# Kernel tuning notes

Hardware: AMD Instinct MI355X
Metric: run time of the kernel (lower is better)

Reference implementation:

```python
import jax, jax.numpy as jnp
import numpy as np


def _softsign(x):
    return x / (1.0 + jnp.abs(x))


def _pad_conv3d(x, w, b):
    # replicate-pad by 1 on each spatial side, then VALID 3x3x3 conv (NCDHW)
    x = jnp.pad(x, ((0, 0), (0, 0), (1, 1), (1, 1), (1, 1)), mode='edge')
    y = jax.lax.conv_general_dilated(
        x, w, window_strides=(1, 1, 1), padding='VALID',
        dimension_numbers=('NCDHW', 'OIDHW', 'NCDHW'))
    return y + b[None, :, None, None, None]


N_MID = 100  # number of 1->1 conv blocks


def setup_inputs() -> dict:
    key = jax.random.key(0)
    ks = jax.random.split(key, 8)
    B, S = 16, 64
    preop = jax.random.normal(ks[0], (B, 1, S, S, S), dtype=jnp.float32)
    intraop = jax.random.normal(ks[1], (B, 1, S, S, S), dtype=jnp.float32)
    # conv weights: PyTorch-style kaiming-ish scale for 3x3x3 kernels
    w0 = jax.random.normal(ks[2], (1, 2, 3, 3, 3), dtype=jnp.float32) * 0.14
    b0 = jax.random.normal(ks[3], (1,), dtype=jnp.float32) * 0.05
    ws = jax.random.normal(ks[4], (N_MID, 1, 1, 3, 3, 3), dtype=jnp.float32) * 0.19
    bs = jax.random.normal(ks[5], (N_MID, 1), dtype=jnp.float32) * 0.05
    wX = jax.random.normal(ks[6], (3, 1, 3, 3, 3), dtype=jnp.float32) * 0.19
    bX = jax.random.normal(ks[7], (3,), dtype=jnp.float32) * 0.05
    return {"preoperative": preop, "intraoperative": intraop,
            "w0": w0, "b0": b0, "ws": ws, "bs": bs, "wX": wX, "bX": bX}


def reference(preoperative, intraoperative, w0, b0, ws, bs, wX, bX):
    config = jnp.concatenate((preoperative, intraoperative), axis=1)  # [B,2,D,H,W]
    h = _softsign(_pad_conv3d(config, w0, b0))  # [B,1,64,64,64]

    def step(h, wb):
        w, b = wb
        return _softsign(_pad_conv3d(h, w, b)), None

    h, _ = jax.lax.scan(step, h, (ws, bs))  # 100 chained 1->1 conv blocks
    res64 = _softsign(_pad_conv3d(h, wX, bX))  # [B,3,64,64,64]
    # torch F.interpolate default mode='nearest': src = floor(dst * in/out)
    res32 = res64[:, :, ::2, ::2, ::2]
    res16 = res64[:, :, ::4, ::4, ::4]
    res8 = res64[:, :, ::8, ::8, ::8]
    return (res64, res32, res16, res8)
```

## Files before the change

### kernel.cpp

```cpp
#include <hip/hip_runtime.h>
#include <math.h>

typedef float f4u __attribute__((ext_vector_type(4), aligned(4)));
typedef float nfloat4 __attribute__((ext_vector_type(4), aligned(16)));
typedef _Float16 h16;
typedef _Float16 h4 __attribute__((ext_vector_type(4)));
typedef _Float16 h2 __attribute__((ext_vector_type(2)));

__device__ __forceinline__ float softsign(float v) {
    float d = 1.0f + fabsf(v);
    return v * __builtin_amdgcn_rcpf(d);
}
__device__ __forceinline__ void nt_store4(float* p, float a, float b, float c, float d) {
    nfloat4 v; v.x = a; v.y = b; v.z = c; v.w = d;
    __builtin_nontemporal_store(v, (nfloat4*)p);
}
__device__ __forceinline__ int clamp63(int v) { return v < 0 ? 0 : (v > 63 ? 63 : v); }

__global__ __launch_bounds__(256) void conv_first(const float* __restrict__ in0,
                                                  const float* __restrict__ in1,
                                                  h16* __restrict__ out,
                                                  const float* __restrict__ w,
                                                  const float* __restrict__ bias) {
    int tid = blockIdx.x * 256 + threadIdx.x;
    int xq = (tid & 15) << 2;
    int y  = (tid >> 4) & 63;
    int z0 = ((tid >> 10) & 15) << 2;
    int b  = tid >> 14;
    const float* base0 = in0 + (size_t)b * 262144;
    const float* base1 = in1 + (size_t)b * 262144;

    float acc[4][4];
    #pragma unroll
    for (int i = 0; i < 4; ++i)
        #pragma unroll
        for (int j = 0; j < 4; ++j) acc[i][j] = 0.0f;

    #pragma unroll
    for (int zi = 0; zi < 6; ++zi) {
        int zin = clamp63(z0 + zi - 1);
        const float* p0 = base0 + zin * 4096;
        const float* p1 = base1 + zin * 4096;
        #pragma unroll
        for (int dy = 0; dy < 3; ++dy) {
            int yin = clamp63(y + dy - 1);
            const float* r0p = p0 + yin * 64;
            const float* r1p = p1 + yin * 64;
            float r0[6], r1[6];
            {
                const float4 v = *(const float4*)(r0p + xq);
                r0[0] = r0p[xq == 0 ? 0 : xq - 1];
                r0[1] = v.x; r0[2] = v.y; r0[3] = v.z; r0[4] = v.w;
                r0[5] = r0p[xq == 60 ? 63 : xq + 4];
            }
            {
                const float4 v = *(const float4*)(r1p + xq);
                r1[0] = r1p[xq == 0 ? 0 : xq - 1];
                r1[1] = v.x; r1[2] = v.y; r1[3] = v.z; r1[4] = v.w;
                r1[5] = r1p[xq == 60 ? 63 : xq + 4];
            }
            #pragma unroll
            for (int dz = 0; dz < 3; ++dz) {
                int zo = zi - dz;
                if (zo >= 0 && zo < 4) {
                    #pragma unroll
                    for (int dx = 0; dx < 3; ++dx) {
                        float w0v = w[dz * 9 + dy * 3 + dx];
                        float w1v = w[27 + dz * 9 + dy * 3 + dx];
                        #pragma unroll
                        for (int xx = 0; xx < 4; ++xx) {
                            acc[zo][xx] = fmaf(w0v, r0[xx + dx], acc[zo][xx]);
                            acc[zo][xx] = fmaf(w1v, r1[xx + dx], acc[zo][xx]);
                        }
                    }
                }
            }
        }
    }
    float bv = *bias;
    h16* obase = out + (size_t)b * 262144 + (size_t)z0 * 4096 + y * 64 + xq;
    #pragma unroll
    for (int zo = 0; zo < 4; ++zo) {
        h4 o;
        o.x = (h16)softsign(acc[zo][0] + bv);
        o.y = (h16)softsign(acc[zo][1] + bv);
        o.z = (h16)softsign(acc[zo][2] + bv);
        o.w = (h16)softsign(acc[zo][3] + bv);
        *(h4*)(obase + zo * 4096) = o;
    }
}

#define LROWH   68
#define LPLANEH 680

__global__ __launch_bounds__(256, 4) void conv_mid(const h16* __restrict__ in,
                                                   h16* __restrict__ out,
                                                   const float* __restrict__ w,
                                                   const float* __restrict__ bias) {
    __shared__ h16 lds[10 * LPLANEH];

    int blk = blockIdx.x;
    int xcd = blk & 7;
    int j   = blk >> 3;
    int b   = j & 15;
    int y0  = ((j >> 4) & 7) << 3;
    int z0  = xcd << 3;

    int t = threadIdx.x;
    int l = t & 15;
    int g = t >> 4;

    const h16* base = in + (size_t)b * 262144;

    float wv[27];
    #pragma unroll
    for (int i = 0; i < 27; ++i) wv[i] = w[i];
    float bv = *bias;

    {
        h16* lrows[7]; h4 mv[7]; h16 tv[7];
        #pragma unroll
        for (int it = 0; it < 7; ++it) {
            int rid = it * 16 + g;
            int pa = rid / 10;
            pa = pa > 9 ? 9 : pa;
            int pr = rid - pa * 10;
            pr = pr > 9 ? 9 : pr;
            const h16* grow = base + clamp63(z0 - 1 + pa) * 4096 + clamp63(y0 - 1 + pr) * 64;
            lrows[it] = &lds[pa * LPLANEH + pr * LROWH];
            mv[it] = *(const h4*)(grow + 4 * l);
            tv[it] = grow[63];
        }
        #pragma unroll
        for (int it = 0; it < 7; ++it) {
            int rid = it * 16 + g;
            if (rid < 100) {
                *(h4*)(lrows[it] + 4 * l) = mv[it];
                if (l == 15) { h2 d; d.x = tv[it]; d.y = tv[it]; *(h2*)(lrows[it] + 64) = d; }
            }
        }
    }
    __syncthreads();

    int xq   = l << 2;
    int yloc = g & 7;
    int zh   = (g >> 3) << 2;

    float acc[4][4];
    #pragma unroll
    for (int i = 0; i < 4; ++i)
        #pragma unroll
        for (int k = 0; k < 4; ++k) acc[i][k] = 0.0f;

    #pragma unroll
    for (int pp = 0; pp < 6; ++pp) {
        const h16* pl = &lds[(zh + pp) * LPLANEH];
        #pragma unroll
        for (int dy = 0; dy < 3; ++dy) {
            const h16* lrow = pl + (yloc + dy) * LROWH;
            h4 v  = *(const h4*)(lrow + xq);
            h2 v2 = *(const h2*)(lrow + xq + 4);
            h2 vf = *(const h2*)(lrow + (xq == 0 ? 0 : xq - 2));
            float r[6];
            r[0] = (xq == 0) ? (float)v.x : (float)vf.y;
            r[1] = (float)v.x; r[2] = (float)v.y; r[3] = (float)v.z;
            r[4] = (float)v.w; r[5] = (float)v2.x;
            #pragma unroll
            for (int dz = 0; dz < 3; ++dz) {
                int zz = pp - dz;
                if (zz >= 0 && zz < 4) {
                    #pragma unroll
                    for (int dx = 0; dx < 3; ++dx) {
                        float ww = wv[dz * 9 + dy * 3 + dx];
                        #pragma unroll
                        for (int xx = 0; xx < 4; ++xx)
                            acc[zz][xx] = fmaf(ww, r[xx + dx], acc[zz][xx]);
                    }
                }
            }
        }
    }

    int y = y0 + yloc;
    h16* obase = out + (size_t)b * 262144 + (size_t)(z0 + zh) * 4096 + y * 64 + xq;
    #pragma unroll
    for (int zz = 0; zz < 4; ++zz) {
        h4 o;
        o.x = (h16)softsign(acc[zz][0] + bv);
        o.y = (h16)softsign(acc[zz][1] + bv);
        o.z = (h16)softsign(acc[zz][2] + bv);
        o.w = (h16)softsign(acc[zz][3] + bv);
        *(h4*)(obase + zz * 4096) = o;
    }
}

__device__ __forceinline__ void load_row6h(const h16* __restrict__ row, int x0, float r[6]) {
    h4 v = *(const h4*)(row + x0);
    r[0] = (float)row[x0 == 0 ? 0 : x0 - 1];
    r[1] = (float)v.x; r[2] = (float)v.y; r[3] = (float)v.z; r[4] = (float)v.w;
    r[5] = (float)row[x0 == 60 ? 63 : x0 + 4];
}

__global__ __launch_bounds__(256) void conv_last(const h16* __restrict__ in,
                                                 float* __restrict__ out,
                                                 const float* __restrict__ w,
                                                 const float* __restrict__ bias) {
    int tid = blockIdx.x * 256 + threadIdx.x;
    int xq = (tid & 15) << 2;
    int y  = (tid >> 4) & 63;
    int z0 = ((tid >> 10) & 15) << 2;
    int b  = tid >> 14;
    const h16* base = in + (size_t)b * 262144;

    float acc[4][3][4];
    #pragma unroll
    for (int i = 0; i < 4; ++i)
        #pragma unroll
        for (int c = 0; c < 3; ++c)
            #pragma unroll
            for (int j = 0; j < 4; ++j) acc[i][c][j] = 0.0f;

    #pragma unroll
    for (int zi = 0; zi < 6; ++zi) {
        int zin = clamp63(z0 + zi - 1);
        const h16* plane = base + zin * 4096;
        #pragma unroll
        for (int dy = 0; dy < 3; ++dy) {
            int yin = clamp63(y + dy - 1);
            float r[6];
            load_row6h(plane + yin * 64, xq, r);
            #pragma unroll
            for (int dz = 0; dz < 3; ++dz) {
                int zo = zi - dz;
                if (zo >= 0 && zo < 4) {
                    #pragma unroll
                    for (int c = 0; c < 3; ++c) {
                        #pragma unroll
                        for (int dx = 0; dx < 3; ++dx) {
                            float wc = w[c * 27 + dz * 9 + dy * 3 + dx];
                            #pragma unroll
                            for (int xx = 0; xx < 4; ++xx)
                                acc[zo][c][xx] = fmaf(wc, r[xx + dx], acc[zo][c][xx]);
                        }
                    }
                }
            }
        }
    }

    float* r64 = out;
    float* r32 = out + 12582912;
    float* r16 = r32 + 1572864;
    float* r8  = r16 + 196608;

    float vals[4][3][4];
    #pragma unroll
    for (int zo = 0; zo < 4; ++zo)
        #pragma unroll
        for (int c = 0; c < 3; ++c) {
            float bv = bias[c];
            #pragma unroll
            for (int xx = 0; xx < 4; ++xx)
                vals[zo][c][xx] = softsign(acc[zo][c][xx] + bv);
        }

    #pragma unroll
    for (int c = 0; c < 3; ++c) {
        float* cb = r64 + ((size_t)b * 3 + c) * 262144 + (size_t)z0 * 4096 + y * 64 + xq;
        #pragma unroll
        for (int zo = 0; zo < 4; ++zo) {
            nt_store4(cb + zo * 4096,
                      vals[zo][c][0], vals[zo][c][1], vals[zo][c][2], vals[zo][c][3]);
        }
    }
    if ((y & 1) == 0) {
        #pragma unroll
        for (int c = 0; c < 3; ++c) {
            size_t cb = ((size_t)b * 3 + c) * 32768 + (size_t)(y >> 1) * 32;
            #pragma unroll
            for (int zo = 0; zo < 4; zo += 2) {
                size_t zb = cb + (size_t)((z0 + zo) >> 1) * 1024;
                __builtin_nontemporal_store(vals[zo][c][0], r32 + zb + ((xq + 0) >> 1));
                __builtin_nontemporal_store(vals[zo][c][2], r32 + zb + ((xq + 2) >> 1));
            }
        }
    }
    if ((y & 3) == 0) {
        #pragma unroll
        for (int c = 0; c < 3; ++c) {
            __builtin_nontemporal_store(vals[0][c][0],
                r16 + ((size_t)b * 3 + c) * 4096 + (size_t)(z0 >> 2) * 256 + (y >> 2) * 16 + (xq >> 2));
        }
    }
    if ((y & 7) == 0 && (z0 & 7) == 0 && (xq & 7) == 0) {
        #pragma unroll
        for (int c = 0; c < 3; ++c) {
            __builtin_nontemporal_store(vals[0][c][0],
                r8 + ((size_t)b * 3 + c) * 512 + (size_t)(z0 >> 3) * 64 + (y >> 3) * 8 + (xq >> 3));
        }
    }
}

extern "C" void kernel_launch(void* const* d_in, const int* in_sizes, int n_in,
                              void* d_out, int out_size, void* d_ws, size_t ws_size,
                              hipStream_t stream) {
    const float* preop = (const float*)d_in[0];
    const float* intra = (const float*)d_in[1];
    const float* w0    = (const float*)d_in[2];
    const float* b0p   = (const float*)d_in[3];
    const float* wsp   = (const float*)d_in[4];
    const float* bsp   = (const float*)d_in[5];
    const float* wX    = (const float*)d_in[6];
    const float* bX    = (const float*)d_in[7];
    float* out = (float*)d_out;

    h16* buf0 = (h16*)d_ws;
    h16* buf1 = (h16*)out;

    conv_first<<<dim3(1024), dim3(256), 0, stream>>>(preop, intra, buf0, w0, b0p);
    for (int i = 0; i < 100; ++i) {
        const h16* src = (i & 1) ? buf1 : buf0;
        h16* dst       = (i & 1) ? buf0 : buf1;
        conv_mid<<<dim3(1024), dim3(256), 0, stream>>>(src, dst, wsp + i * 27, bsp + i);
    }
    conv_last<<<dim3(1024), dim3(256), 0, stream>>>(buf0, out, wX, bX);
}
```

Measured before the change: 944.6 us.

## Process two y-tiles per conv_mid block, prefetching the second tile's halo into registers

Each conv_mid block now handles two 8-row y tiles instead of one, so the grid is halved to 512 blocks. The global loads for both tiles are issued up front. The second tile's data waits in registers and is written to a second LDS buffer after the first tile's compute, so its load latency is hidden behind that compute. This raises register and LDS use: launch bounds drop to 2 blocks per CU and there are fewer blocks in flight, which can lower occupancy and load balance.

```diff
diff --git a/kernel.cpp b/kernel.cpp
--- a/kernel.cpp
+++ b/kernel.cpp
@@ -93,55 +93,11 @@
 #define LROWH   68
 #define LPLANEH 680
 
-__global__ __launch_bounds__(256, 4) void conv_mid(const h16* __restrict__ in,
-                                                   h16* __restrict__ out,
-                                                   const float* __restrict__ w,
-                                                   const float* __restrict__ bias) {
-    __shared__ h16 lds[10 * LPLANEH];
-
-    int blk = blockIdx.x;
-    int xcd = blk & 7;
-    int j   = blk >> 3;
-    int b   = j & 15;
-    int y0  = ((j >> 4) & 7) << 3;
-    int z0  = xcd << 3;
-
-    int t = threadIdx.x;
-    int l = t & 15;
-    int g = t >> 4;
-
-    const h16* base = in + (size_t)b * 262144;
-
-    float wv[27];
-    #pragma unroll
-    for (int i = 0; i < 27; ++i) wv[i] = w[i];
-    float bv = *bias;
-
-    {
-        h16* lrows[7]; h4 mv[7]; h16 tv[7];
-        #pragma unroll
-        for (int it = 0; it < 7; ++it) {
-            int rid = it * 16 + g;
-            int pa = rid / 10;
-            pa = pa > 9 ? 9 : pa;
-            int pr = rid - pa * 10;
-            pr = pr > 9 ? 9 : pr;
-            const h16* grow = base + clamp63(z0 - 1 + pa) * 4096 + clamp63(y0 - 1 + pr) * 64;
-            lrows[it] = &lds[pa * LPLANEH + pr * LROWH];
-            mv[it] = *(const h4*)(grow + 4 * l);
-            tv[it] = grow[63];
-        }
-        #pragma unroll
-        for (int it = 0; it < 7; ++it) {
-            int rid = it * 16 + g;
-            if (rid < 100) {
-                *(h4*)(lrows[it] + 4 * l) = mv[it];
-                if (l == 15) { h2 d; d.x = tv[it]; d.y = tv[it]; *(h2*)(lrows[it] + 64) = d; }
-            }
-        }
-    }
-    __syncthreads();
-
+__device__ __forceinline__ void mid_compute_tile(const h16* __restrict__ ldsbuf,
+                                                 h16* __restrict__ out,
+                                                 const float wv[27], float bv,
+                                                 size_t bofs, int z0, int y0,
+                                                 int l, int g) {
     int xq   = l << 2;
     int yloc = g & 7;
     int zh   = (g >> 3) << 2;
@@ -154,7 +110,7 @@
 
     #pragma unroll
     for (int pp = 0; pp < 6; ++pp) {
-        const h16* pl = &lds[(zh + pp) * LPLANEH];
+        const h16* pl = &ldsbuf[(zh + pp) * LPLANEH];
         #pragma unroll
         for (int dy = 0; dy < 3; ++dy) {
             const h16* lrow = pl + (yloc + dy) * LROWH;
@@ -182,7 +138,7 @@
     }
 
     int y = y0 + yloc;
-    h16* obase = out + (size_t)b * 262144 + (size_t)(z0 + zh) * 4096 + y * 64 + xq;
+    h16* obase = out + bofs + (size_t)(z0 + zh) * 4096 + y * 64 + xq;
     #pragma unroll
     for (int zz = 0; zz < 4; ++zz) {
         h4 o;
@@ -192,6 +148,74 @@
         o.w = (h16)softsign(acc[zz][3] + bv);
         *(h4*)(obase + zz * 4096) = o;
     }
+}
+
+__global__ __launch_bounds__(256, 2) void conv_mid(const h16* __restrict__ in,
+                                                   h16* __restrict__ out,
+                                                   const float* __restrict__ w,
+                                                   const float* __restrict__ bias) {
+    __shared__ h16 lds[2][10 * LPLANEH];
+
+    int blk = blockIdx.x;
+    int xcd = blk & 7;
+    int j   = blk >> 3;
+    int b   = j & 15;
+    int y0p = ((j >> 4) & 3) << 4;
+    int z0  = xcd << 3;
+
+    int t = threadIdx.x;
+    int l = t & 15;
+    int g = t >> 4;
+
+    const size_t bofs = (size_t)b * 262144;
+    const h16* base = in + bofs;
+
+    float wv[27];
+    #pragma unroll
+    for (int i = 0; i < 27; ++i) wv[i] = w[i];
+    float bv = *bias;
+
+    h16* lrows[2][7]; h4 mv[2][7]; h16 tv[2][7];
+    #pragma unroll
+    for (int tt = 0; tt < 2; ++tt) {
+        int y0 = y0p + tt * 8;
+        #pragma unroll
+        for (int it = 0; it < 7; ++it) {
+            int rid = it * 16 + g;
+            int pa = rid / 10;
+            pa = pa > 9 ? 9 : pa;
+            int pr = rid - pa * 10;
+            pr = pr > 9 ? 9 : pr;
+            const h16* grow = base + clamp63(z0 - 1 + pa) * 4096 + clamp63(y0 - 1 + pr) * 64;
+            lrows[tt][it] = &lds[tt][pa * LPLANEH + pr * LROWH];
+            mv[tt][it] = *(const h4*)(grow + 4 * l);
+            tv[tt][it] = grow[63];
+        }
+    }
+
+    #pragma unroll
+    for (int it = 0; it < 7; ++it) {
+        int rid = it * 16 + g;
+        if (rid < 100) {
+            *(h4*)(lrows[0][it] + 4 * l) = mv[0][it];
+            if (l == 15) { h2 d; d.x = tv[0][it]; d.y = tv[0][it]; *(h2*)(lrows[0][it] + 64) = d; }
+        }
+    }
+    __syncthreads();
+
+    mid_compute_tile(lds[0], out, wv, bv, bofs, z0, y0p, l, g);
+
+    #pragma unroll
+    for (int it = 0; it < 7; ++it) {
+        int rid = it * 16 + g;
+        if (rid < 100) {
+            *(h4*)(lrows[1][it] + 4 * l) = mv[1][it];
+            if (l == 15) { h2 d; d.x = tv[1][it]; d.y = tv[1][it]; *(h2*)(lrows[1][it] + 64) = d; }
+        }
+    }
+    __syncthreads();
+
+    mid_compute_tile(lds[1], out, wv, bv, bofs, z0, y0p + 8, l, g);
 }
 
 __device__ __forceinline__ void load_row6h(const h16* __restrict__ row, int x0, float r[6]) {
@@ -321,7 +345,7 @@
     for (int i = 0; i < 100; ++i) {
         const h16* src = (i & 1) ? buf1 : buf0;
         h16* dst       = (i & 1) ? buf0 : buf1;
-        conv_mid<<<dim3(1024), dim3(256), 0, stream>>>(src, dst, wsp + i * 27, bsp + i);
+        conv_mid<<<dim3(512), dim3(256), 0, stream>>>(src, dst, wsp + i * 27, bsp + i);
     }
     conv_last<<<dim3(1024), dim3(256), 0, stream>>>(buf0, out, wX, bX);
 }
```

New measurement: 1.037 ms. 9.7% more time.

## Fuse pairs of chained 3D conv layers into one kernel with halo recompute

Applied to the files above, without the earlier changes.

Each launch now applies two consecutive 1->1 conv+softsign layers, so the launch count drops from 100 to 50. The first layer is computed over a 10x10-row halo region in shared memory from a 12x12-row staged input tile; the second layer then reads that intermediate with replicate-clamped indexing. This halves global reads and writes of the intermediate volume and the per-launch overhead. In exchange it recomputes halo rows (about 1.56x the work for the first layer), leaves 6 of 16 thread groups idle during stage one, and raises shared memory and register pressure (a 40-float accumulator per thread).

```diff
diff --git a/kernel.cpp b/kernel.cpp
--- a/kernel.cpp
+++ b/kernel.cpp
@@ -1,7 +1,6 @@
 #include <hip/hip_runtime.h>
 #include <math.h>
 
-typedef float f4u __attribute__((ext_vector_type(4), aligned(4)));
 typedef float nfloat4 __attribute__((ext_vector_type(4), aligned(16)));
 typedef _Float16 h16;
 typedef _Float16 h4 __attribute__((ext_vector_type(4)));
@@ -90,14 +89,17 @@
     }
 }
 
-#define LROWH   68
-#define LPLANEH 680
-
-__global__ __launch_bounds__(256, 4) void conv_mid(const h16* __restrict__ in,
-                                                   h16* __restrict__ out,
-                                                   const float* __restrict__ w,
-                                                   const float* __restrict__ bias) {
-    __shared__ h16 lds[10 * LPLANEH];
+#define SPLH 816
+#define MPLH 680
+
+__global__ __launch_bounds__(256, 4) void conv_mid2(const h16* __restrict__ in,
+                                                    h16* __restrict__ out,
+                                                    const float* __restrict__ w1,
+                                                    const float* __restrict__ w2,
+                                                    const float* __restrict__ b1,
+                                                    const float* __restrict__ b2) {
+    __shared__ h16 sA[12 * SPLH];
+    __shared__ h16 sM[10 * MPLH];
 
     int blk = blockIdx.x;
     int xcd = blk & 7;
@@ -110,87 +112,150 @@
     int l = t & 15;
     int g = t >> 4;
 
-    const h16* base = in + (size_t)b * 262144;
-
-    float wv[27];
-    #pragma unroll
-    for (int i = 0; i < 27; ++i) wv[i] = w[i];
-    float bv = *bias;
+    const size_t bofs = (size_t)b * 262144;
+    const h16* base = in + bofs;
 
     {
-        h16* lrows[7]; h4 mv[7]; h16 tv[7];
-        #pragma unroll
-        for (int it = 0; it < 7; ++it) {
+        h16* lrows[9]; h4 mv[9]; h16 tv[9];
+        #pragma unroll
+        for (int it = 0; it < 9; ++it) {
             int rid = it * 16 + g;
-            int pa = rid / 10;
-            pa = pa > 9 ? 9 : pa;
-            int pr = rid - pa * 10;
-            pr = pr > 9 ? 9 : pr;
-            const h16* grow = base + clamp63(z0 - 1 + pa) * 4096 + clamp63(y0 - 1 + pr) * 64;
-            lrows[it] = &lds[pa * LPLANEH + pr * LROWH];
+            int pa = rid / 12;
+            int pr = rid - pa * 12;
+            const h16* grow = base + clamp63(z0 - 2 + pa) * 4096 + clamp63(y0 - 2 + pr) * 64;
+            lrows[it] = &sA[pa * SPLH + pr * 68];
             mv[it] = *(const h4*)(grow + 4 * l);
             tv[it] = grow[63];
         }
         #pragma unroll
-        for (int it = 0; it < 7; ++it) {
-            int rid = it * 16 + g;
-            if (rid < 100) {
-                *(h4*)(lrows[it] + 4 * l) = mv[it];
-                if (l == 15) { h2 d; d.x = tv[it]; d.y = tv[it]; *(h2*)(lrows[it] + 64) = d; }
-            }
+        for (int it = 0; it < 9; ++it) {
+            *(h4*)(lrows[it] + 4 * l) = mv[it];
+            if (l == 15) { h2 d; d.x = tv[it]; d.y = tv[it]; *(h2*)(lrows[it] + 64) = d; }
         }
     }
     __syncthreads();
 
-    int xq   = l << 2;
-    int yloc = g & 7;
-    int zh   = (g >> 3) << 2;
-
-    float acc[4][4];
-    #pragma unroll
-    for (int i = 0; i < 4; ++i)
-        #pragma unroll
-        for (int k = 0; k < 4; ++k) acc[i][k] = 0.0f;
-
-    #pragma unroll
-    for (int pp = 0; pp < 6; ++pp) {
-        const h16* pl = &lds[(zh + pp) * LPLANEH];
-        #pragma unroll
-        for (int dy = 0; dy < 3; ++dy) {
-            const h16* lrow = pl + (yloc + dy) * LROWH;
-            h4 v  = *(const h4*)(lrow + xq);
-            h2 v2 = *(const h2*)(lrow + xq + 4);
-            h2 vf = *(const h2*)(lrow + (xq == 0 ? 0 : xq - 2));
-            float r[6];
-            r[0] = (xq == 0) ? (float)v.x : (float)vf.y;
-            r[1] = (float)v.x; r[2] = (float)v.y; r[3] = (float)v.z;
-            r[4] = (float)v.w; r[5] = (float)v2.x;
-            #pragma unroll
-            for (int dz = 0; dz < 3; ++dz) {
-                int zz = pp - dz;
-                if (zz >= 0 && zz < 4) {
+    {
+        int l2 = t & 15;
+        int r  = t >> 4;
+        if (r < 10) {
+            float wv1[27];
+            #pragma unroll
+            for (int i = 0; i < 27; ++i) wv1[i] = w1[i];
+            float b1v = *b1;
+            int xq2 = l2 << 2;
+
+            float acc[10][4];
+            #pragma unroll
+            for (int i = 0; i < 10; ++i)
+                #pragma unroll
+                for (int k = 0; k < 4; ++k) acc[i][k] = b1v;
+
+            #pragma unroll
+            for (int pa = 0; pa < 12; ++pa) {
+                #pragma unroll
+                for (int dy = 0; dy < 3; ++dy) {
+                    const h16* lrow = &sA[pa * SPLH + (r + dy) * 68];
+                    h4 v  = *(const h4*)(lrow + xq2);
+                    h2 v2 = *(const h2*)(lrow + xq2 + 4);
+                    h2 vf = *(const h2*)(lrow + (xq2 == 0 ? 0 : xq2 - 2));
+                    float rr[6];
+                    rr[0] = (xq2 == 0) ? (float)v.x : (float)vf.y;
+                    rr[1] = (float)v.x; rr[2] = (float)v.y; rr[3] = (float)v.z;
+                    rr[4] = (float)v.w; rr[5] = (float)v2.x;
                     #pragma unroll
-                    for (int dx = 0; dx < 3; ++dx) {
-                        float ww = wv[dz * 9 + dy * 3 + dx];
-                        #pragma unroll
-                        for (int xx = 0; xx < 4; ++xx)
-                            acc[zz][xx] = fmaf(ww, r[xx + dx], acc[zz][xx]);
+                    for (int dz = 0; dz < 3; ++dz) {
+                        int pi = pa - dz;
+                        if (pi >= 0 && pi < 10) {
+                            #pragma unroll
+                            for (int dx = 0; dx < 3; ++dx) {
+                                float ww = wv1[dz * 9 + dy * 3 + dx];
+                                #pragma unroll
+                                for (int xx = 0; xx < 4; ++xx)
+                                    acc[pi][xx] = fmaf(ww, rr[xx + dx], acc[pi][xx]);
+                            }
+                        }
                     }
                 }
             }
-        }
-    }
-
-    int y = y0 + yloc;
-    h16* obase = out + (size_t)b * 262144 + (size_t)(z0 + zh) * 4096 + y * 64 + xq;
-    #pragma unroll
-    for (int zz = 0; zz < 4; ++zz) {
-        h4 o;
-        o.x = (h16)softsign(acc[zz][0] + bv);
-        o.y = (h16)softsign(acc[zz][1] + bv);
-        o.z = (h16)softsign(acc[zz][2] + bv);
-        o.w = (h16)softsign(acc[zz][3] + bv);
-        *(h4*)(obase + zz * 4096) = o;
+            #pragma unroll
+            for (int pi = 0; pi < 10; ++pi) {
+                h4 o;
+                o.x = (h16)softsign(acc[pi][0]);
+                o.y = (h16)softsign(acc[pi][1]);
+                o.z = (h16)softsign(acc[pi][2]);
+                o.w = (h16)softsign(acc[pi][3]);
+                h16* orow = &sM[pi * MPLH + r * 68];
+                *(h4*)(orow + xq2) = o;
+                if (l2 == 15) { h2 d; d.x = o.w; d.y = o.w; *(h2*)(orow + 64) = d; }
+            }
+        }
+    }
+    __syncthreads();
+
+    {
+        float wv2[27];
+        #pragma unroll
+        for (int i = 0; i < 27; ++i) wv2[i] = w2[i];
+        float b2v = *b2;
+
+        int xq   = l << 2;
+        int yloc = g & 7;
+        int zh   = (g >> 3) << 2;
+
+        int zsl[6];
+        #pragma unroll
+        for (int k = 0; k < 6; ++k) zsl[k] = clamp63(z0 + zh + k - 1) - z0 + 1;
+        int sc[3];
+        #pragma unroll
+        for (int dy = 0; dy < 3; ++dy) sc[dy] = clamp63(y0 + yloc + dy - 1) - y0 + 1;
+
+        float acc[4][4];
+        #pragma unroll
+        for (int i = 0; i < 4; ++i)
+            #pragma unroll
+            for (int k = 0; k < 4; ++k) acc[i][k] = b2v;
+
+        #pragma unroll
+        for (int pp = 0; pp < 6; ++pp) {
+            const h16* pl = &sM[zsl[pp] * MPLH];
+            #pragma unroll
+            for (int dy = 0; dy < 3; ++dy) {
+                const h16* lrow = pl + sc[dy] * 68;
+                h4 v  = *(const h4*)(lrow + xq);
+                h2 v2 = *(const h2*)(lrow + xq + 4);
+                h2 vf = *(const h2*)(lrow + (xq == 0 ? 0 : xq - 2));
+                float rr[6];
+                rr[0] = (xq == 0) ? (float)v.x : (float)vf.y;
+                rr[1] = (float)v.x; rr[2] = (float)v.y; rr[3] = (float)v.z;
+                rr[4] = (float)v.w; rr[5] = (float)v2.x;
+                #pragma unroll
+                for (int dz = 0; dz < 3; ++dz) {
+                    int zz = pp - dz;
+                    if (zz >= 0 && zz < 4) {
+                        #pragma unroll
+                        for (int dx = 0; dx < 3; ++dx) {
+                            float ww = wv2[dz * 9 + dy * 3 + dx];
+                            #pragma unroll
+                            for (int xx = 0; xx < 4; ++xx)
+                                acc[zz][xx] = fmaf(ww, rr[xx + dx], acc[zz][xx]);
+                        }
+                    }
+                }
+            }
+        }
+
+        int y = y0 + yloc;
+        h16* obase = out + bofs + (size_t)(z0 + zh) * 4096 + y * 64 + xq;
+        #pragma unroll
+        for (int zz = 0; zz < 4; ++zz) {
+            h4 o;
+            o.x = (h16)softsign(acc[zz][0]);
+            o.y = (h16)softsign(acc[zz][1]);
+            o.z = (h16)softsign(acc[zz][2]);
+            o.w = (h16)softsign(acc[zz][3]);
+            *(h4*)(obase + zz * 4096) = o;
+        }
     }
 }
 
@@ -318,10 +383,14 @@
     h16* buf1 = (h16*)out;
 
     conv_first<<<dim3(1024), dim3(256), 0, stream>>>(preop, intra, buf0, w0, b0p);
-    for (int i = 0; i < 100; ++i) {
-        const h16* src = (i & 1) ? buf1 : buf0;
-        h16* dst       = (i & 1) ? buf0 : buf1;
-        conv_mid<<<dim3(1024), dim3(256), 0, stream>>>(src, dst, wsp + i * 27, bsp + i);
+    for (int k = 0; k < 50; ++k) {
+        const h16* src = (k & 1) ? buf1 : buf0;
+        h16* dst       = (k & 1) ? buf0 : buf1;
+        conv_mid2<<<dim3(1024), dim3(256), 0, stream>>>(src, dst,
+                                                        wsp + (2 * k) * 27,
+                                                        wsp + (2 * k + 1) * 27,
+                                                        bsp + 2 * k,
+                                                        bsp + 2 * k + 1);
     }
     conv_last<<<dim3(1024), dim3(256), 0, stream>>>(buf0, out, wX, bX);
 }
```

Measured after the change: 1.517 ms. 60.6% more time.
